# Kernel tuning notes

Hardware: AMD Instinct MI355X
Metric: run time of the kernel (lower is better)

Reference implementation:

```python
import jax, jax.numpy as jnp
import numpy as np

N = 8192
F_IN, HID, LAT = 256, 128, 32


def setup_inputs() -> dict:
    key = jax.random.key(0)
    k1, k2, k3, k4 = jax.random.split(key, 4)
    X = jax.random.normal(k1, (N, F_IN), dtype=jnp.float32)
    # Dense normalized-adjacency stand-in (original converts dense A_tilde to COO each call)
    A_tilde = jax.random.uniform(k2, (N, N), dtype=jnp.float32) / N
    # Xavier-uniform init like torch's init.xavier_uniform_ on Linear weights
    lim1 = float(np.sqrt(6.0 / (F_IN + HID)))
    lim2 = float(np.sqrt(6.0 / (HID + LAT)))
    W1 = jax.random.uniform(k3, (F_IN, HID), dtype=jnp.float32, minval=-lim1, maxval=lim1)
    W2 = jax.random.uniform(k4, (HID, LAT), dtype=jnp.float32, minval=-lim2, maxval=lim2)
    return {"X": X, "A_tilde": A_tilde, "W1": W1, "W2": W2}


def reference(X, A_tilde, W1, W2):
    # GCN layer 1: A_tilde @ (X W1), then ReLU
    h = jax.nn.relu(A_tilde @ (X @ W1))          # [N, HID]
    # GCN layer 2 (no activation)
    Z = A_tilde @ (h @ W2)                        # [N, LAT]
    # Inner-product decoder
    A_hat = jax.nn.sigmoid(Z @ Z.T)               # [N, N]
    return A_hat
```

## Files before the change

kernel.cpp:

```cpp
#include <hip/hip_runtime.h>
#include <hip/hip_bf16.h>

#define N_ 8192
#define F_ 256
#define H_ 128
#define L_ 32

typedef __attribute__((ext_vector_type(8))) short bf16x8;
typedef __attribute__((ext_vector_type(4))) float f32x4;
typedef __attribute__((ext_vector_type(4))) short bf16x4;

__device__ __forceinline__ unsigned f2bf_u(float x) {
    unsigned u = __builtin_bit_cast(unsigned, x);
    return (u + 0x7fffu + ((u >> 16) & 1u)) >> 16;
}
__device__ __forceinline__ short f2bf(float x) { return (short)f2bf_u(x); }

__device__ __forceinline__ bf16x8 cvt8(float4 a, float4 b) {
    bf16x8 v;
    v[0] = f2bf(a.x); v[1] = f2bf(a.y); v[2] = f2bf(a.z); v[3] = f2bf(a.w);
    v[4] = f2bf(b.x); v[5] = f2bf(b.y); v[6] = f2bf(b.z); v[7] = f2bf(b.w);
    return v;
}

__global__ __launch_bounds__(256) void k0_cvt(const float* __restrict__ A,
                                              short* __restrict__ Ab) {
    size_t g = ((size_t)blockIdx.x * 256 + threadIdx.x) * 8;
    float4 a = *(const float4*)(A + g);
    float4 b = *(const float4*)(A + g + 4);
    *(bf16x8*)(Ab + g) = cvt8(a, b);
}

__global__ __launch_bounds__(256) void k1_xw1(const float* __restrict__ X,
                                              const float* __restrict__ W1,
                                              short* __restrict__ XW1T) {
    __shared__ short w1t[H_ * (F_ + 8)];
    const int tid = threadIdx.x;
    for (int idx = tid; idx < F_ * H_; idx += 256) {
        int k = idx >> 7, n = idx & 127;
        w1t[n * (F_ + 8) + k] = f2bf(W1[idx]);
    }
    __syncthreads();
    const int wv = tid >> 6, l = tid & 63;
    const int lm = l & 15, q = l >> 4;
    const int i0 = blockIdx.x * 64 + wv * 16;
    const float* xrow = X + (size_t)(i0 + lm) * F_;
    f32x4 acc[8];
#pragma unroll
    for (int j = 0; j < 8; ++j) acc[j] = (f32x4){0.f, 0.f, 0.f, 0.f};
#pragma unroll
    for (int k0 = 0; k0 < F_; k0 += 32) {
        float4 a0 = *(const float4*)(xrow + k0 + q * 8);
        float4 a1 = *(const float4*)(xrow + k0 + q * 8 + 4);
        bf16x8 af = cvt8(a0, a1);
#pragma unroll
        for (int j = 0; j < 8; ++j) {
            bf16x8 bf = *(const bf16x8*)&w1t[(j * 16 + lm) * (F_ + 8) + k0 + q * 8];
            acc[j] = __builtin_amdgcn_mfma_f32_16x16x32_bf16(af, bf, acc[j], 0, 0, 0);
        }
    }
#pragma unroll
    for (int j = 0; j < 8; ++j) {
        bf16x4 o;
        o[0] = f2bf(acc[j][0]); o[1] = f2bf(acc[j][1]);
        o[2] = f2bf(acc[j][2]); o[3] = f2bf(acc[j][3]);
        *(bf16x4*)(XW1T + (size_t)(j * 16 + lm) * N_ + i0 + q * 4) = o;
    }
}

__global__ __launch_bounds__(256) void k2_h_zp(const short* __restrict__ Ab,
                                               const short* __restrict__ XW1T,
                                               const float* __restrict__ W2,
                                               short* __restrict__ ZPT) {
    __shared__ float lacc[4][16][132];
    __shared__ short hl[16][136];
    __shared__ short w2t[32][136];
    const int tid = threadIdx.x;
    for (int idx = tid; idx < H_ * L_; idx += 256) {
        int k = idx >> 5, j = idx & 31;
        w2t[j][k] = f2bf(W2[idx]);
    }
    const int wv = tid >> 6, l = tid & 63, lm = l & 15, q = l >> 4;
    const int i0 = blockIdx.x * 16;
    const int kbeg = wv * (N_ / 4);
    const short* Arow = Ab + (size_t)(i0 + lm) * N_ + kbeg + q * 8;
    const short* Bp[8];
#pragma unroll
    for (int jt = 0; jt < 8; ++jt)
        Bp[jt] = XW1T + (size_t)(jt * 16 + lm) * N_ + kbeg + q * 8;

    bf16x8 pa[2], pb[2][8];
#pragma unroll
    for (int t = 0; t < 2; ++t) {
        pa[t] = *(const bf16x8*)(Arow + t * 32);
#pragma unroll
        for (int jt = 0; jt < 8; ++jt) pb[t][jt] = *(const bf16x8*)(Bp[jt] + t * 32);
    }
    f32x4 acc[8];
#pragma unroll
    for (int j = 0; j < 8; ++j) acc[j] = (f32x4){0.f, 0.f, 0.f, 0.f};

    const int NS = (N_ / 4) / 32;
#pragma unroll 2
    for (int s = 0; s < NS; ++s) {
        const int p = s & 1;
        bf16x8 af = pa[p];
#pragma unroll
        for (int jt = 0; jt < 8; ++jt)
            acc[jt] = __builtin_amdgcn_mfma_f32_16x16x32_bf16(af, pb[p][jt], acc[jt], 0, 0, 0);
        if (s + 2 < NS) {
            pa[p] = *(const bf16x8*)(Arow + (s + 2) * 32);
#pragma unroll
            for (int jt = 0; jt < 8; ++jt)
                pb[p][jt] = *(const bf16x8*)(Bp[jt] + (s + 2) * 32);
        }
    }
#pragma unroll
    for (int jt = 0; jt < 8; ++jt)
#pragma unroll
        for (int r = 0; r < 4; ++r)
            lacc[wv][q * 4 + r][jt * 16 + lm] = acc[jt][r];
    __syncthreads();
    for (int e = tid; e < 16 * H_; e += 256) {
        int rr = e >> 7, c = e & 127;
        float v = (lacc[0][rr][c] + lacc[1][rr][c]) + (lacc[2][rr][c] + lacc[3][rr][c]);
        hl[rr][c] = f2bf(v > 0.f ? v : 0.f);
    }
    __syncthreads();
    if (wv < 2) {
        f32x4 a2 = (f32x4){0.f, 0.f, 0.f, 0.f};
#pragma unroll
        for (int k0 = 0; k0 < H_; k0 += 32) {
            bf16x8 af2 = *(const bf16x8*)&hl[lm][k0 + q * 8];
            bf16x8 bf2 = *(const bf16x8*)&w2t[wv * 16 + lm][k0 + q * 8];
            a2 = __builtin_amdgcn_mfma_f32_16x16x32_bf16(af2, bf2, a2, 0, 0, 0);
        }
        bf16x4 o;
        o[0] = f2bf(a2[0]); o[1] = f2bf(a2[1]); o[2] = f2bf(a2[2]); o[3] = f2bf(a2[3]);
        *(bf16x4*)(ZPT + (size_t)(wv * 16 + lm) * N_ + i0 + q * 4) = o;
    }
}

__global__ __launch_bounds__(256) void k3_z(const short* __restrict__ Ab,
                                            const short* __restrict__ ZPT,
                                            short* __restrict__ Z) {
    __shared__ float lacc[4][16][36];
    const int tid = threadIdx.x;
    const int wv = tid >> 6, l = tid & 63, lm = l & 15, q = l >> 4;
    const int i0 = blockIdx.x * 16;
    const int kbeg = wv * (N_ / 4);
    const short* Arow = Ab + (size_t)(i0 + lm) * N_ + kbeg + q * 8;
    const short* Bp0 = ZPT + (size_t)lm * N_ + kbeg + q * 8;
    const short* Bp1 = Bp0 + (size_t)16 * N_;

    bf16x8 pa[2], pb0[2], pb1[2];
#pragma unroll
    for (int t = 0; t < 2; ++t) {
        pa[t]  = *(const bf16x8*)(Arow + t * 32);
        pb0[t] = *(const bf16x8*)(Bp0 + t * 32);
        pb1[t] = *(const bf16x8*)(Bp1 + t * 32);
    }
    f32x4 acc0 = (f32x4){0.f, 0.f, 0.f, 0.f};
    f32x4 acc1 = (f32x4){0.f, 0.f, 0.f, 0.f};
    const int NS = (N_ / 4) / 32;
#pragma unroll 2
    for (int s = 0; s < NS; ++s) {
        const int p = s & 1;
        acc0 = __builtin_amdgcn_mfma_f32_16x16x32_bf16(pa[p], pb0[p], acc0, 0, 0, 0);
        acc1 = __builtin_amdgcn_mfma_f32_16x16x32_bf16(pa[p], pb1[p], acc1, 0, 0, 0);
        if (s + 2 < NS) {
            pa[p]  = *(const bf16x8*)(Arow + (s + 2) * 32);
            pb0[p] = *(const bf16x8*)(Bp0 + (s + 2) * 32);
            pb1[p] = *(const bf16x8*)(Bp1 + (s + 2) * 32);
        }
    }
#pragma unroll
    for (int r = 0; r < 4; ++r) {
        lacc[wv][q * 4 + r][lm]      = acc0[r];
        lacc[wv][q * 4 + r][16 + lm] = acc1[r];
    }
    __syncthreads();
    {
        int e = tid * 2;
        int rr = e >> 5, c = e & 31;
        float v0 = (lacc[0][rr][c] + lacc[1][rr][c]) + (lacc[2][rr][c] + lacc[3][rr][c]);
        float v1 = (lacc[0][rr][c + 1] + lacc[1][rr][c + 1]) + (lacc[2][rr][c + 1] + lacc[3][rr][c + 1]);
        unsigned pk = f2bf_u(v0) | (f2bf_u(v1) << 16);
        *(unsigned*)(Z + (size_t)(i0 + rr) * L_ + c) = pk;
    }
}

__global__ __launch_bounds__(256) void k4_dec(const short* __restrict__ Z,
                                              float* __restrict__ out) {
    __shared__ float os[128][132];
    const int tid = threadIdx.x;
    const int wv = tid >> 6, l = tid & 63;
    const int lm = l & 15, q = l >> 4;
    const int bj = blockIdx.x & 63, bi = blockIdx.x >> 6;
    const int i0 = bi * 128, j0 = bj * 128;
    bf16x8 af[2];
#pragma unroll
    for (int t = 0; t < 2; ++t)
        af[t] = *(const bf16x8*)(Z + (size_t)(i0 + wv * 32 + t * 16 + lm) * L_ + q * 8);
#pragma unroll
    for (int tj = 0; tj < 8; ++tj) {
        bf16x8 bfv = *(const bf16x8*)(Z + (size_t)(j0 + tj * 16 + lm) * L_ + q * 8);
#pragma unroll
        for (int t = 0; t < 2; ++t) {
            f32x4 c = __builtin_amdgcn_mfma_f32_16x16x32_bf16(
                af[t], bfv, (f32x4){0.f, 0.f, 0.f, 0.f}, 0, 0, 0);
#pragma unroll
            for (int r = 0; r < 4; ++r) {
                float e = __expf(-c[r]);
                os[wv * 32 + t * 16 + q * 4 + r][tj * 16 + lm] = __fdividef(1.f, 1.f + e);
            }
        }
    }
    __syncthreads();
    for (int idx = tid; idx < 128 * 32; idx += 256) {
        int row = idx >> 5, c4 = idx & 31;
        *(float4*)(out + (size_t)(i0 + row) * N_ + j0 + c4 * 4) = *(const float4*)&os[row][c4 * 4];
    }
}

extern "C" void kernel_launch(void* const* d_in, const int* in_sizes, int n_in,
                              void* d_out, int out_size, void* d_ws, size_t ws_size,
                              hipStream_t stream) {
    const float* X  = (const float*)d_in[0];
    const float* A  = (const float*)d_in[1];
    const float* W1 = (const float*)d_in[2];
    const float* W2 = (const float*)d_in[3];
    float* out = (float*)d_out;

    short* XW1T = (short*)d_ws;
    short* ZPT  = XW1T + (size_t)H_ * N_;
    short* Z    = ZPT + (size_t)L_ * N_;
    short* Ab   = Z + (size_t)N_ * L_;

    k1_xw1<<<N_ / 64, 256, 0, stream>>>(X, W1, XW1T);
    k0_cvt<<<(N_ * N_) / (256 * 8), 256, 0, stream>>>(A, Ab);
    k2_h_zp<<<N_ / 16, 256, 0, stream>>>(Ab, XW1T, W2, ZPT);
    k3_z<<<N_ / 16, 256, 0, stream>>>(Ab, ZPT, Z);
    k4_dec<<<(N_ / 128) * (N_ / 128), 256, 0, stream>>>(Z, out);
}
```

Before: 672.9 us.

## Read fp32 adjacency directly in LDS-tiled split-K GEMMs, drop bf16 copy

Removes the separate pass that converted the full N×N adjacency to bf16. Both propagation GEMMs now load fp32 A tiles, convert them in registers and stage them into double-buffered LDS tiles. Each 64-row block is split four ways along K, with partial sums written to global scratch and reduced in small follow-up kernels (k2b fuses ReLU and the W2 projection). This saves one write and one read of the bf16 matrix but reads fp32 A twice instead of bf16 A twice, and adds partial-sum traffic and extra launches.

```diff
diff --git a/kernel.cpp b/kernel.cpp
--- a/kernel.cpp
+++ b/kernel.cpp
@@ -5,6 +5,9 @@
 #define F_ 256
 #define H_ 128
 #define L_ 32
+#define TK 64
+#define KQN 4
+#define KQL (N_ / KQN)
 
 typedef __attribute__((ext_vector_type(8))) short bf16x8;
 typedef __attribute__((ext_vector_type(4))) float f32x4;
@@ -16,6 +19,11 @@
 }
 __device__ __forceinline__ short f2bf(float x) { return (short)f2bf_u(x); }
 
+__device__ __forceinline__ bf16x4 cvt4(float4 a) {
+    bf16x4 v;
+    v[0] = f2bf(a.x); v[1] = f2bf(a.y); v[2] = f2bf(a.z); v[3] = f2bf(a.w);
+    return v;
+}
 __device__ __forceinline__ bf16x8 cvt8(float4 a, float4 b) {
     bf16x8 v;
     v[0] = f2bf(a.x); v[1] = f2bf(a.y); v[2] = f2bf(a.z); v[3] = f2bf(a.w);
@@ -23,14 +31,6 @@
     return v;
 }
 
-__global__ __launch_bounds__(256) void k0_cvt(const float* __restrict__ A,
-                                              short* __restrict__ Ab) {
-    size_t g = ((size_t)blockIdx.x * 256 + threadIdx.x) * 8;
-    float4 a = *(const float4*)(A + g);
-    float4 b = *(const float4*)(A + g + 4);
-    *(bf16x8*)(Ab + g) = cvt8(a, b);
-}
-
 __global__ __launch_bounds__(256) void k1_xw1(const float* __restrict__ X,
                                               const float* __restrict__ W1,
                                               short* __restrict__ XW1T) {
@@ -68,126 +68,184 @@
     }
 }
 
-__global__ __launch_bounds__(256) void k2_h_zp(const short* __restrict__ Ab,
-                                               const short* __restrict__ XW1T,
-                                               const float* __restrict__ W2,
-                                               short* __restrict__ ZPT) {
-    __shared__ float lacc[4][16][132];
-    __shared__ short hl[16][136];
+__global__ __launch_bounds__(512) void k2a(const float* __restrict__ A,
+                                           const short* __restrict__ XW1T,
+                                           float* __restrict__ P4) {
+    __shared__ short As[2][64][72];
+    __shared__ short Bs[2][128][72];
+    const int tid = threadIdx.x;
+    const int bi = blockIdx.x >> 2, kq = blockIdx.x & 3;
+    const int i0 = bi * 64, kbase = kq * KQL;
+    const int ar = tid >> 4, ac = (tid & 15) * 4;
+    const int br = tid >> 3, bc = (tid & 7) * 8;
+    const float* Ap = A + (size_t)(i0 + ar) * N_ + kbase + ac;
+    const short* Bp = XW1T + (size_t)br * N_ + kbase + bc;
+
+    const int wv = tid >> 6, l = tid & 63, lm = l & 15, q = l >> 4;
+    const int rg = wv & 3, ch = wv >> 2;
+
+    float4 pa0, pa1; bf16x8 pb0, pb1;
+#define LOADG(s) do { size_t o = (size_t)(s) * TK; \
+        pa0 = *(const float4*)(Ap + o); \
+        pa1 = *(const float4*)(Ap + o + (size_t)32 * N_); \
+        pb0 = *(const bf16x8*)(Bp + o); \
+        pb1 = *(const bf16x8*)(Bp + o + (size_t)64 * N_); } while (0)
+#define STORES(b) do { \
+        *(bf16x4*)&As[b][ar][ac] = cvt4(pa0); \
+        *(bf16x4*)&As[b][ar + 32][ac] = cvt4(pa1); \
+        *(bf16x8*)&Bs[b][br][bc] = pb0; \
+        *(bf16x8*)&Bs[b][br + 64][bc] = pb1; } while (0)
+
+    LOADG(0); STORES(0); LOADG(1);
+    __syncthreads();
+
+    f32x4 acc[4];
+#pragma unroll
+    for (int j = 0; j < 4; ++j) acc[j] = (f32x4){0.f, 0.f, 0.f, 0.f};
+    const int NS = KQL / TK;
+#pragma unroll 2
+    for (int s = 0; s < NS; ++s) {
+        const int b = s & 1;
+#pragma unroll
+        for (int kh = 0; kh < 2; ++kh) {
+            bf16x8 af = *(const bf16x8*)&As[b][rg * 16 + lm][kh * 32 + q * 8];
+#pragma unroll
+            for (int jt = 0; jt < 4; ++jt) {
+                bf16x8 bfv = *(const bf16x8*)&Bs[b][ch * 64 + jt * 16 + lm][kh * 32 + q * 8];
+                acc[jt] = __builtin_amdgcn_mfma_f32_16x16x32_bf16(af, bfv, acc[jt], 0, 0, 0);
+            }
+        }
+        if (s + 1 < NS) {
+            STORES((s + 1) & 1);
+            if (s + 2 < NS) LOADG(s + 2);
+        }
+        __syncthreads();
+    }
+#undef LOADG
+#undef STORES
+    float* Pb = P4 + ((size_t)kq * N_ + i0 + rg * 16 + q * 4) * H_ + ch * 64 + lm;
+#pragma unroll
+    for (int jt = 0; jt < 4; ++jt)
+#pragma unroll
+        for (int r = 0; r < 4; ++r)
+            Pb[(size_t)r * H_ + jt * 16] = acc[jt][r];
+}
+
+__global__ __launch_bounds__(256) void k2b(const float* __restrict__ P4,
+                                           const float* __restrict__ W2,
+                                           short* __restrict__ ZPT) {
+    __shared__ short hl[32][136];
     __shared__ short w2t[32][136];
     const int tid = threadIdx.x;
     for (int idx = tid; idx < H_ * L_; idx += 256) {
         int k = idx >> 5, j = idx & 31;
         w2t[j][k] = f2bf(W2[idx]);
     }
+    const int i0 = blockIdx.x * 32;
+    const int r = tid >> 3, c16 = (tid & 7) * 16;
+    float4 v[4];
+#pragma unroll
+    for (int cc = 0; cc < 4; ++cc) v[cc] = (float4){0.f, 0.f, 0.f, 0.f};
+#pragma unroll
+    for (int kq = 0; kq < 4; ++kq) {
+        const float* p = P4 + ((size_t)kq * N_ + i0 + r) * H_ + c16;
+#pragma unroll
+        for (int cc = 0; cc < 4; ++cc) {
+            float4 t = *(const float4*)(p + cc * 4);
+            v[cc].x += t.x; v[cc].y += t.y; v[cc].z += t.z; v[cc].w += t.w;
+        }
+    }
+#pragma unroll
+    for (int cc = 0; cc < 4; ++cc) {
+        v[cc].x = v[cc].x > 0.f ? v[cc].x : 0.f;
+        v[cc].y = v[cc].y > 0.f ? v[cc].y : 0.f;
+        v[cc].z = v[cc].z > 0.f ? v[cc].z : 0.f;
+        v[cc].w = v[cc].w > 0.f ? v[cc].w : 0.f;
+    }
+    *(bf16x8*)&hl[r][c16] = cvt8(v[0], v[1]);
+    *(bf16x8*)&hl[r][c16 + 8] = cvt8(v[2], v[3]);
+    __syncthreads();
     const int wv = tid >> 6, l = tid & 63, lm = l & 15, q = l >> 4;
-    const int i0 = blockIdx.x * 16;
-    const int kbeg = wv * (N_ / 4);
-    const short* Arow = Ab + (size_t)(i0 + lm) * N_ + kbeg + q * 8;
-    const short* Bp[8];
-#pragma unroll
-    for (int jt = 0; jt < 8; ++jt)
-        Bp[jt] = XW1T + (size_t)(jt * 16 + lm) * N_ + kbeg + q * 8;
-
-    bf16x8 pa[2], pb[2][8];
-#pragma unroll
-    for (int t = 0; t < 2; ++t) {
-        pa[t] = *(const bf16x8*)(Arow + t * 32);
-#pragma unroll
-        for (int jt = 0; jt < 8; ++jt) pb[t][jt] = *(const bf16x8*)(Bp[jt] + t * 32);
-    }
-    f32x4 acc[8];
-#pragma unroll
-    for (int j = 0; j < 8; ++j) acc[j] = (f32x4){0.f, 0.f, 0.f, 0.f};
-
-    const int NS = (N_ / 4) / 32;
+    const int ti = wv & 1, tj = wv >> 1;
+    f32x4 a2 = (f32x4){0.f, 0.f, 0.f, 0.f};
+#pragma unroll
+    for (int k0 = 0; k0 < H_; k0 += 32) {
+        bf16x8 af = *(const bf16x8*)&hl[ti * 16 + lm][k0 + q * 8];
+        bf16x8 bf = *(const bf16x8*)&w2t[tj * 16 + lm][k0 + q * 8];
+        a2 = __builtin_amdgcn_mfma_f32_16x16x32_bf16(af, bf, a2, 0, 0, 0);
+    }
+    bf16x4 o;
+    o[0] = f2bf(a2[0]); o[1] = f2bf(a2[1]); o[2] = f2bf(a2[2]); o[3] = f2bf(a2[3]);
+    *(bf16x4*)(ZPT + (size_t)(tj * 16 + lm) * N_ + i0 + ti * 16 + q * 4) = o;
+}
+
+__global__ __launch_bounds__(512) void k3a(const float* __restrict__ A,
+                                           const short* __restrict__ ZPT,
+                                           float* __restrict__ Q4) {
+    __shared__ short As[2][64][72];
+    __shared__ short Bs[2][32][72];
+    const int tid = threadIdx.x;
+    const int bi = blockIdx.x >> 2, kq = blockIdx.x & 3;
+    const int i0 = bi * 64, kbase = kq * KQL;
+    const int ar = tid >> 4, ac = (tid & 15) * 4;
+    const int br = tid >> 4, bc = (tid & 15) * 4;
+    const float* Ap = A + (size_t)(i0 + ar) * N_ + kbase + ac;
+    const short* Bp = ZPT + (size_t)br * N_ + kbase + bc;
+
+    const int wv = tid >> 6, l = tid & 63, lm = l & 15, q = l >> 4;
+    const int rg = wv & 3, ch = wv >> 2;
+
+    float4 pa0, pa1; bf16x4 pb0;
+#define LOADG(s) do { size_t o = (size_t)(s) * TK; \
+        pa0 = *(const float4*)(Ap + o); \
+        pa1 = *(const float4*)(Ap + o + (size_t)32 * N_); \
+        pb0 = *(const bf16x4*)(Bp + o); } while (0)
+#define STORES(b) do { \
+        *(bf16x4*)&As[b][ar][ac] = cvt4(pa0); \
+        *(bf16x4*)&As[b][ar + 32][ac] = cvt4(pa1); \
+        *(bf16x4*)&Bs[b][br][bc] = pb0; } while (0)
+
+    LOADG(0); STORES(0); LOADG(1);
+    __syncthreads();
+
+    f32x4 acc = (f32x4){0.f, 0.f, 0.f, 0.f};
+    const int NS = KQL / TK;
 #pragma unroll 2
     for (int s = 0; s < NS; ++s) {
-        const int p = s & 1;
-        bf16x8 af = pa[p];
-#pragma unroll
-        for (int jt = 0; jt < 8; ++jt)
-            acc[jt] = __builtin_amdgcn_mfma_f32_16x16x32_bf16(af, pb[p][jt], acc[jt], 0, 0, 0);
-        if (s + 2 < NS) {
-            pa[p] = *(const bf16x8*)(Arow + (s + 2) * 32);
-#pragma unroll
-            for (int jt = 0; jt < 8; ++jt)
-                pb[p][jt] = *(const bf16x8*)(Bp[jt] + (s + 2) * 32);
-        }
-    }
-#pragma unroll
-    for (int jt = 0; jt < 8; ++jt)
-#pragma unroll
-        for (int r = 0; r < 4; ++r)
-            lacc[wv][q * 4 + r][jt * 16 + lm] = acc[jt][r];
-    __syncthreads();
-    for (int e = tid; e < 16 * H_; e += 256) {
-        int rr = e >> 7, c = e & 127;
-        float v = (lacc[0][rr][c] + lacc[1][rr][c]) + (lacc[2][rr][c] + lacc[3][rr][c]);
-        hl[rr][c] = f2bf(v > 0.f ? v : 0.f);
-    }
-    __syncthreads();
-    if (wv < 2) {
-        f32x4 a2 = (f32x4){0.f, 0.f, 0.f, 0.f};
-#pragma unroll
-        for (int k0 = 0; k0 < H_; k0 += 32) {
-            bf16x8 af2 = *(const bf16x8*)&hl[lm][k0 + q * 8];
-            bf16x8 bf2 = *(const bf16x8*)&w2t[wv * 16 + lm][k0 + q * 8];
-            a2 = __builtin_amdgcn_mfma_f32_16x16x32_bf16(af2, bf2, a2, 0, 0, 0);
-        }
-        bf16x4 o;
-        o[0] = f2bf(a2[0]); o[1] = f2bf(a2[1]); o[2] = f2bf(a2[2]); o[3] = f2bf(a2[3]);
-        *(bf16x4*)(ZPT + (size_t)(wv * 16 + lm) * N_ + i0 + q * 4) = o;
-    }
-}
-
-__global__ __launch_bounds__(256) void k3_z(const short* __restrict__ Ab,
-                                            const short* __restrict__ ZPT,
-                                            short* __restrict__ Z) {
-    __shared__ float lacc[4][16][36];
-    const int tid = threadIdx.x;
-    const int wv = tid >> 6, l = tid & 63, lm = l & 15, q = l >> 4;
-    const int i0 = blockIdx.x * 16;
-    const int kbeg = wv * (N_ / 4);
-    const short* Arow = Ab + (size_t)(i0 + lm) * N_ + kbeg + q * 8;
-    const short* Bp0 = ZPT + (size_t)lm * N_ + kbeg + q * 8;
-    const short* Bp1 = Bp0 + (size_t)16 * N_;
-
-    bf16x8 pa[2], pb0[2], pb1[2];
-#pragma unroll
-    for (int t = 0; t < 2; ++t) {
-        pa[t]  = *(const bf16x8*)(Arow + t * 32);
-        pb0[t] = *(const bf16x8*)(Bp0 + t * 32);
-        pb1[t] = *(const bf16x8*)(Bp1 + t * 32);
-    }
-    f32x4 acc0 = (f32x4){0.f, 0.f, 0.f, 0.f};
-    f32x4 acc1 = (f32x4){0.f, 0.f, 0.f, 0.f};
-    const int NS = (N_ / 4) / 32;
-#pragma unroll 2
-    for (int s = 0; s < NS; ++s) {
-        const int p = s & 1;
-        acc0 = __builtin_amdgcn_mfma_f32_16x16x32_bf16(pa[p], pb0[p], acc0, 0, 0, 0);
-        acc1 = __builtin_amdgcn_mfma_f32_16x16x32_bf16(pa[p], pb1[p], acc1, 0, 0, 0);
-        if (s + 2 < NS) {
-            pa[p]  = *(const bf16x8*)(Arow + (s + 2) * 32);
-            pb0[p] = *(const bf16x8*)(Bp0 + (s + 2) * 32);
-            pb1[p] = *(const bf16x8*)(Bp1 + (s + 2) * 32);
-        }
-    }
-#pragma unroll
-    for (int r = 0; r < 4; ++r) {
-        lacc[wv][q * 4 + r][lm]      = acc0[r];
-        lacc[wv][q * 4 + r][16 + lm] = acc1[r];
-    }
-    __syncthreads();
-    {
-        int e = tid * 2;
-        int rr = e >> 5, c = e & 31;
-        float v0 = (lacc[0][rr][c] + lacc[1][rr][c]) + (lacc[2][rr][c] + lacc[3][rr][c]);
-        float v1 = (lacc[0][rr][c + 1] + lacc[1][rr][c + 1]) + (lacc[2][rr][c + 1] + lacc[3][rr][c + 1]);
-        unsigned pk = f2bf_u(v0) | (f2bf_u(v1) << 16);
-        *(unsigned*)(Z + (size_t)(i0 + rr) * L_ + c) = pk;
-    }
+        const int b = s & 1;
+#pragma unroll
+        for (int kh = 0; kh < 2; ++kh) {
+            bf16x8 af = *(const bf16x8*)&As[b][rg * 16 + lm][kh * 32 + q * 8];
+            bf16x8 bfv = *(const bf16x8*)&Bs[b][ch * 16 + lm][kh * 32 + q * 8];
+            acc = __builtin_amdgcn_mfma_f32_16x16x32_bf16(af, bfv, acc, 0, 0, 0);
+        }
+        if (s + 1 < NS) {
+            STORES((s + 1) & 1);
+            if (s + 2 < NS) LOADG(s + 2);
+        }
+        __syncthreads();
+    }
+#undef LOADG
+#undef STORES
+    float* Qb = Q4 + ((size_t)kq * N_ + i0 + rg * 16 + q * 4) * L_ + ch * 16 + lm;
+#pragma unroll
+    for (int r = 0; r < 4; ++r)
+        Qb[(size_t)r * L_] = acc[r];
+}
+
+__global__ __launch_bounds__(256) void k3b(const float* __restrict__ Q4,
+                                           short* __restrict__ Z) {
+    size_t g = ((size_t)blockIdx.x * 256 + threadIdx.x) * 8;
+    float4 s0 = (float4){0.f, 0.f, 0.f, 0.f}, s1 = s0;
+#pragma unroll
+    for (int kq = 0; kq < 4; ++kq) {
+        const float* p = Q4 + (size_t)kq * N_ * L_ + g;
+        float4 a = *(const float4*)(p);
+        float4 b = *(const float4*)(p + 4);
+        s0.x += a.x; s0.y += a.y; s0.z += a.z; s0.w += a.w;
+        s1.x += b.x; s1.y += b.y; s1.z += b.z; s1.w += b.w;
+    }
+    *(bf16x8*)(Z + g) = cvt8(s0, s1);
 }
 
 __global__ __launch_bounds__(256) void k4_dec(const short* __restrict__ Z,
@@ -235,11 +293,13 @@
     short* XW1T = (short*)d_ws;
     short* ZPT  = XW1T + (size_t)H_ * N_;
     short* Z    = ZPT + (size_t)L_ * N_;
-    short* Ab   = Z + (size_t)N_ * L_;
+    float* P4   = (float*)(Z + (size_t)N_ * L_);
+    float* Q4   = P4 + (size_t)4 * N_ * H_;
 
     k1_xw1<<<N_ / 64, 256, 0, stream>>>(X, W1, XW1T);
-    k0_cvt<<<(N_ * N_) / (256 * 8), 256, 0, stream>>>(A, Ab);
-    k2_h_zp<<<N_ / 16, 256, 0, stream>>>(Ab, XW1T, W2, ZPT);
-    k3_z<<<N_ / 16, 256, 0, stream>>>(Ab, ZPT, Z);
+    k2a<<<(N_ / 64) * KQN, 512, 0, stream>>>(A, XW1T, P4);
+    k2b<<<N_ / 32, 256, 0, stream>>>(P4, W2, ZPT);
+    k3a<<<(N_ / 64) * KQN, 512, 0, stream>>>(A, ZPT, Q4);
+    k3b<<<(N_ * L_) / (256 * 8), 256, 0, stream>>>(Q4, Z);
     k4_dec<<<(N_ / 128) * (N_ / 128), 256, 0, stream>>>(Z, out);
 }
```

Measured after the change: 561.0 us. 16.6% less time.
